# Performance work log

Measured on AMD Instinct MI355X. Metric: run time of the kernel, lower is better.

Reference implementation:

```python
import jax, jax.numpy as jnp
import numpy as np

N_HEAD = 4
D_K = 64
D_V = 64
D_MODEL = 256
LN_EPS = 1e-5


def setup_inputs() -> dict:
    key = jax.random.key(0)
    k1, k2, k3 = jax.random.split(key, 3)
    B, C, H, W = 2, D_MODEL, 64, 64
    q = jax.random.normal(k1, (B, C, H, W), dtype=jnp.float32)
    # w_qkvs: Linear(d_model, n_head*d_k, bias=False), weight [out, in]
    std_qkv = np.sqrt(2.0 / (D_MODEL + D_K))
    w_qkv = jax.random.normal(k2, (N_HEAD * D_K, D_MODEL), dtype=jnp.float32) * std_qkv
    # fc: Linear(n_head*d_v, d_model), xavier-normal-ish init
    std_fc = np.sqrt(2.0 / (N_HEAD * D_V + D_MODEL))
    fc_w = jax.random.normal(k3, (D_MODEL, N_HEAD * D_V), dtype=jnp.float32) * std_fc
    fc_b = jnp.zeros((D_MODEL,), dtype=jnp.float32)
    ln_g = jnp.ones((D_MODEL,), dtype=jnp.float32)
    ln_b = jnp.zeros((D_MODEL,), dtype=jnp.float32)
    return {"q": q, "w_qkv": w_qkv, "fc_w": fc_w, "fc_b": fc_b, "ln_g": ln_g, "ln_b": ln_b}


def reference(q, w_qkv, fc_w, fc_b, ln_g, ln_b):
    B, C, H, W = q.shape
    L = H * W
    # [B, C, H, W] -> [B, L, C]
    x = q.reshape(B, C, L).transpose(0, 2, 1)
    residual = x
    # shared QKV projection (self-attention branch: q == k == v)
    qkv = x @ w_qkv.T                                  # [B, L, nh*dk]
    qh = qkv.reshape(B, L, N_HEAD, D_K).transpose(2, 0, 1, 3)  # [h, B, L, dk]
    scale = jnp.asarray(np.sqrt(D_K), dtype=q.dtype)
    attn = jnp.einsum('hbqd,hbkd->hbqk', qh, qh) / scale       # [h, B, L, L]
    attn = jax.nn.softmax(attn, axis=-1)
    out = jnp.einsum('hbqk,hbkd->hbqd', attn, qh)              # [h, B, L, dv]
    # [h, B, L, dv] -> [B, L, h*dv]
    out = out.transpose(1, 2, 0, 3).reshape(B, L, N_HEAD * D_V)
    out = out @ fc_w.T + fc_b
    out = out + residual
    mu = jnp.mean(out, axis=-1, keepdims=True)
    var = jnp.mean(jnp.square(out - mu), axis=-1, keepdims=True)
    out = (out - mu) / jnp.sqrt(var + LN_EPS) * ln_g + ln_b
    # raw row-major view back to [B, C, H, W] (matches torch .view)
    return out.reshape(B, -1, H, W)
```

## Files before the change

### kernel.cpp

```cpp
#include <hip/hip_runtime.h>

#define L_SEQ 4096
#define DMODEL 256
#define DH 64
#define NKB 16

typedef __attribute__((ext_vector_type(8))) __bf16 bf16x8;
typedef __attribute__((ext_vector_type(4))) float f32x4;
typedef __attribute__((ext_vector_type(8))) unsigned short ushort8v;
typedef __attribute__((ext_vector_type(4))) unsigned short ushort4v;

__device__ __forceinline__ unsigned short f2bf(float f) {
  unsigned u = __builtin_bit_cast(unsigned, f);
  u += 0x7fffu + ((u >> 16) & 1u);
  return (unsigned short)(u >> 16);
}
__device__ __forceinline__ float bf2f(unsigned short h) {
  unsigned u = ((unsigned)h) << 16;
  return __builtin_bit_cast(float, u);
}
__device__ __forceinline__ bf16x8 ld_frag(const unsigned short* p) {
  return __builtin_bit_cast(bf16x8, *(const ushort8v*)p);
}

__global__ __launch_bounds__(256) void k_transpose(const float* __restrict__ q,
                                                   unsigned short* __restrict__ xbf,
                                                   const float* __restrict__ w,
                                                   const float* __restrict__ fcw,
                                                   unsigned short* __restrict__ wbf,
                                                   unsigned short* __restrict__ fcwbf) {
  int bx = blockIdx.x;
  int t = threadIdx.x;
  if (bx >= 512) {
    int i = ((bx - 512) * 256 + t) * 4;
    float4 a = *(const float4*)(w + i);
    float4 b = *(const float4*)(fcw + i);
    ushort4v av = {f2bf(a.x), f2bf(a.y), f2bf(a.z), f2bf(a.w)};
    ushort4v bv = {f2bf(b.x), f2bf(b.y), f2bf(b.z), f2bf(b.w)};
    *(ushort4v*)(wbf + i) = av;
    *(ushort4v*)(fcwbf + i) = bv;
    return;
  }
  __shared__ float T[64 * 65];
  int b = bx >> 8, rest = bx & 255;
  int ct = rest >> 6, lt = rest & 63;
#pragma unroll
  for (int it = 0; it < 4; ++it) {
    int i = (t >> 4) + it * 16;
    int j0 = (t & 15) * 4;
    float4 v = *(const float4*)(q + ((size_t)(b * 256 + ct * 64 + i)) * 4096 + lt * 64 + j0);
    T[i * 65 + j0 + 0] = v.x;
    T[i * 65 + j0 + 1] = v.y;
    T[i * 65 + j0 + 2] = v.z;
    T[i * 65 + j0 + 3] = v.w;
  }
  __syncthreads();
#pragma unroll
  for (int it = 0; it < 2; ++it) {
    int l = (t >> 3) + it * 32;
    int c0 = (t & 7) * 8;
    ushort8v o;
#pragma unroll
    for (int k = 0; k < 8; ++k) o[k] = f2bf(T[(c0 + k) * 65 + l]);
    *(ushort8v*)(xbf + ((size_t)(b * 4096 + lt * 64 + l)) * 256 + ct * 64 + c0) = o;
  }
}

#define KP2 136
__global__ __launch_bounds__(256) void k_qkv(const unsigned short* __restrict__ xbf,
                                             const unsigned short* __restrict__ wbf,
                                             unsigned short* __restrict__ Qh,
                                             unsigned short* __restrict__ QhT) {
  __shared__ unsigned short As[64 * KP2];
  __shared__ unsigned short Bs[64 * KP2];
  int bx = blockIdx.x;
  int mtile = bx >> 2, h = bx & 3;
  int m0 = mtile * 64;
  int b = m0 >> 12, l0 = m0 & 4095;
  int t = threadIdx.x;
  int wv = t >> 6, lane = t & 63, g = lane >> 4, ln = lane & 15;
  f32x4 acc[4] = {};
  for (int kb = 0; kb < 2; ++kb) {
#pragma unroll
    for (int it = 0; it < 4; ++it) {
      int idx = t + it * 256;
      int row = idx >> 4;
      int c0 = (idx & 15) * 8;
      *(ushort8v*)(As + row * KP2 + c0) =
          *(const ushort8v*)(xbf + (size_t)(m0 + row) * 256 + kb * 128 + c0);
      *(ushort8v*)(Bs + row * KP2 + c0) =
          *(const ushort8v*)(wbf + (size_t)(h * 64 + row) * 256 + kb * 128 + c0);
    }
    __syncthreads();
#pragma unroll
    for (int kc = 0; kc < 4; ++kc) {
      bf16x8 a = ld_frag(As + (wv * 16 + ln) * KP2 + kc * 32 + g * 8);
#pragma unroll
      for (int tn = 0; tn < 4; ++tn) {
        bf16x8 bb = ld_frag(Bs + (tn * 16 + ln) * KP2 + kc * 32 + g * 8);
        acc[tn] = __builtin_amdgcn_mfma_f32_16x16x32_bf16(a, bb, acc[tn], 0, 0, 0);
      }
    }
    __syncthreads();
  }
  size_t pbase = (size_t)(b * 4 + h);
#pragma unroll
  for (int tn = 0; tn < 4; ++tn) {
#pragma unroll
    for (int r = 0; r < 4; ++r) {
      int lrow = wv * 16 + g * 4 + r;
      int d = tn * 16 + ln;
      unsigned short bv = f2bf(acc[tn][r]);
      As[lrow * 64 + (((d >> 3) ^ (lrow & 7)) * 8) + (d & 7)] = bv;
      Bs[d * 64 + (((lrow >> 3) ^ (d & 7)) * 8) + (lrow & 7)] = bv;
    }
  }
#pragma unroll
  for (int s = 0; s < 2; ++s) {
    int flat = s * 64 + lane;
    int lrow = wv * 16 + (flat >> 3);
    int c8 = lane & 7;
    ushort8v v = *(const ushort8v*)(As + lrow * 64 + ((c8 ^ (lrow & 7)) * 8));
    *(ushort8v*)(Qh + (pbase * L_SEQ + l0 + lrow) * DH + c8 * 8) = v;
  }
  __syncthreads();
#pragma unroll
  for (int s = 0; s < 2; ++s) {
    int flat = s * 256 + t;
    int drow = flat >> 3;
    int c8 = t & 7;
    ushort8v v = *(const ushort8v*)(Bs + drow * 64 + ((c8 ^ (drow & 7)) * 8));
    *(ushort8v*)(QhT + (pbase * DH + drow) * L_SEQ + l0 + c8 * 8) = v;
  }
}

__global__ __launch_bounds__(256, 2) void k_attn(const unsigned short* __restrict__ Qh,
                                                 const unsigned short* __restrict__ QhT,
                                                 unsigned short* __restrict__ Opart,
                                                 float* __restrict__ Lpart) {
  __shared__ unsigned short Kt[64 * 64];
  __shared__ unsigned short Vt[64 * 64];
  __shared__ unsigned short Pb[256 * 64];
  int bx = blockIdx.x;
  int p = bx & 7;
  int u = bx >> 3;
  int qsup = u & 15, ks = u >> 4;
  int t = threadIdx.x;
  int wv = t >> 6, lane = t & 63, g = lane >> 4, ln = lane & 15;
  const unsigned short* Qp = Qh + (size_t)p * L_SEQ * DH;
  const unsigned short* QTp = QhT + (size_t)p * DH * L_SEQ;
  int q0 = qsup * 256;
  int qw = q0 + wv * 64;

  bf16x8 aQ[4][2];
#pragma unroll
  for (int nt = 0; nt < 4; ++nt)
#pragma unroll
    for (int kc = 0; kc < 2; ++kc)
      aQ[nt][kc] = ld_frag(Qp + (size_t)(qw + nt * 16 + ln) * DH + kc * 32 + g * 8);

  f32x4 oacc[4][4] = {};
  float lacc[4] = {0.f, 0.f, 0.f, 0.f};

  int srow0 = t >> 3, scol0 = t & 7;
  int srow1 = (t + 256) >> 3, scol1 = (t + 256) & 7;
  int sdst0 = srow0 * 64 + ((scol0 ^ (srow0 & 7)) * 8);
  int sdst1 = srow1 * 64 + ((scol1 ^ (srow1 & 7)) * 8);

  ushort8v kreg0, kreg1, vreg0, vreg1;
  {
    int kbase = (ks * NKB) * 64;
    kreg0 = *(const ushort8v*)(Qp + (size_t)(kbase + srow0) * DH + scol0 * 8);
    kreg1 = *(const ushort8v*)(Qp + (size_t)(kbase + srow1) * DH + scol1 * 8);
    vreg0 = *(const ushort8v*)(QTp + (size_t)srow0 * L_SEQ + kbase + scol0 * 8);
    vreg1 = *(const ushort8v*)(QTp + (size_t)srow1 * L_SEQ + kbase + scol1 * 8);
  }

  for (int kb = 0; kb < NKB; ++kb) {
    __syncthreads();
    *(ushort8v*)(Kt + sdst0) = kreg0;
    *(ushort8v*)(Kt + sdst1) = kreg1;
    *(ushort8v*)(Vt + sdst0) = vreg0;
    *(ushort8v*)(Vt + sdst1) = vreg1;
    __syncthreads();
    if (kb + 1 < NKB) {
      int kbase = (ks * NKB + kb + 1) * 64;
      kreg0 = *(const ushort8v*)(Qp + (size_t)(kbase + srow0) * DH + scol0 * 8);
      kreg1 = *(const ushort8v*)(Qp + (size_t)(kbase + srow1) * DH + scol1 * 8);
      vreg0 = *(const ushort8v*)(QTp + (size_t)srow0 * L_SEQ + kbase + scol0 * 8);
      vreg1 = *(const ushort8v*)(QTp + (size_t)srow1 * L_SEQ + kbase + scol1 * 8);
    }
#pragma unroll
    for (int mt = 0; mt < 4; ++mt) {
      int krow = mt * 16 + ln;
      bf16x8 aK0 = ld_frag(Kt + krow * 64 + (((0 * 4 + g) ^ (ln & 7)) * 8));
      bf16x8 aK1 = ld_frag(Kt + krow * 64 + (((1 * 4 + g) ^ (ln & 7)) * 8));
      f32x4 s[4] = {};
#pragma unroll
      for (int nt = 0; nt < 4; ++nt) {
        s[nt] = __builtin_amdgcn_mfma_f32_16x16x32_bf16(aK0, aQ[nt][0], s[nt], 0, 0, 0);
        s[nt] = __builtin_amdgcn_mfma_f32_16x16x32_bf16(aK1, aQ[nt][1], s[nt], 0, 0, 0);
      }
#pragma unroll
      for (int nt = 0; nt < 4; ++nt) {
        float p0 = __expf(fmaf(s[nt][0], 0.125f, -16.0f));
        float p1 = __expf(fmaf(s[nt][1], 0.125f, -16.0f));
        float p2 = __expf(fmaf(s[nt][2], 0.125f, -16.0f));
        float p3 = __expf(fmaf(s[nt][3], 0.125f, -16.0f));
        lacc[nt] += (p0 + p1) + (p2 + p3);
        ushort4v pk = {f2bf(p0), f2bf(p1), f2bf(p2), f2bf(p3)};
        int row = wv * 64 + nt * 16 + ln;
        int addr = row * 64 + (((2 * mt + (g >> 1)) ^ (ln & 7)) * 8) + (g & 1) * 4;
        *(ushort4v*)(Pb + addr) = pk;
      }
    }
#pragma unroll
    for (int kc = 0; kc < 2; ++kc) {
      bf16x8 bV[4];
#pragma unroll
      for (int tn = 0; tn < 4; ++tn)
        bV[tn] = ld_frag(Vt + (tn * 16 + ln) * 64 + (((kc * 4 + g) ^ (ln & 7)) * 8));
#pragma unroll
      for (int mq = 0; mq < 4; ++mq) {
        bf16x8 aP = ld_frag(Pb + (wv * 64 + mq * 16 + ln) * 64 + (((kc * 4 + g) ^ (ln & 7)) * 8));
#pragma unroll
        for (int tn = 0; tn < 4; ++tn)
          oacc[mq][tn] = __builtin_amdgcn_mfma_f32_16x16x32_bf16(aP, bV[tn], oacc[mq][tn], 0, 0, 0);
      }
    }
  }
#pragma unroll
  for (int nt = 0; nt < 4; ++nt) {
    lacc[nt] += __shfl_xor(lacc[nt], 16, 64);
    lacc[nt] += __shfl_xor(lacc[nt], 32, 64);
  }
  size_t pq = (size_t)(ks * 8 + p) * L_SEQ;
  if (g == 0) {
#pragma unroll
    for (int nt = 0; nt < 4; ++nt)
      __builtin_nontemporal_store(lacc[nt], &Lpart[pq + qw + nt * 16 + ln]);
  }
#pragma unroll
  for (int mq = 0; mq < 4; ++mq) {
#pragma unroll
    for (int r = 0; r < 4; ++r) {
      int row = wv * 64 + mq * 16 + g * 4 + r;
#pragma unroll
      for (int tn = 0; tn < 4; ++tn) {
        int d = tn * 16 + ln;
        Pb[row * 64 + (((d >> 3) ^ (row & 7)) * 8) + (d & 7)] = f2bf(oacc[mq][tn][r]);
      }
    }
  }
#pragma unroll
  for (int s = 0; s < 8; ++s) {
    int flat = s * 64 + lane;
    int row = wv * 64 + (flat >> 3);
    int c8 = lane & 7;
    ushort8v v = *(const ushort8v*)(Pb + row * 64 + ((c8 ^ (row & 7)) * 8));
    __builtin_nontemporal_store(v, (ushort8v*)(Opart + (pq + q0 + row) * DH + c8 * 8));
  }
}

#define CP 72
__global__ __launch_bounds__(256) void k_fc(const unsigned short* __restrict__ Opart,
                                            const float* __restrict__ Lpart,
                                            const unsigned short* __restrict__ fcwbf,
                                            const float* __restrict__ qres,
                                            const float* __restrict__ fcb,
                                            const float* __restrict__ lng,
                                            const float* __restrict__ lnb,
                                            float* __restrict__ out) {
  __shared__ unsigned short As[32 * CP];
  __shared__ unsigned short Bs[256 * CP];
  __shared__ float redS[4][32], redQ[4][32], muA[32], rsA[32];
  int bx = blockIdx.x;
  int m0 = bx * 32;
  int b = m0 >> 12, lpart = m0 & 4095;
  int t = threadIdx.x;
  int wv = t >> 6, lane = t & 63, g = lane >> 4, ln = lane & 15;
  f32x4 acc[2][4] = {};
  for (int kb = 0; kb < 4; ++kb) {
    {
      int row = t >> 3, c0 = (t & 7) * 8;
      int q = lpart + row;
      int p = b * 4 + kb;
      float lsum = __builtin_nontemporal_load(&Lpart[(size_t)(0 * 8 + p) * L_SEQ + q]) +
                   __builtin_nontemporal_load(&Lpart[(size_t)(1 * 8 + p) * L_SEQ + q]) +
                   __builtin_nontemporal_load(&Lpart[(size_t)(2 * 8 + p) * L_SEQ + q]) +
                   __builtin_nontemporal_load(&Lpart[(size_t)(3 * 8 + p) * L_SEQ + q]);
      float inv = 1.0f / lsum;
      float a8[8] = {0.f, 0.f, 0.f, 0.f, 0.f, 0.f, 0.f, 0.f};
#pragma unroll
      for (int ksp = 0; ksp < 4; ++ksp) {
        ushort8v v = __builtin_nontemporal_load(
            (const ushort8v*)(Opart + ((size_t)(ksp * 8 + p) * L_SEQ + q) * DH + c0));
#pragma unroll
        for (int j = 0; j < 8; ++j) a8[j] += bf2f(v[j]);
      }
      ushort8v o;
#pragma unroll
      for (int j = 0; j < 8; ++j) o[j] = f2bf(a8[j] * inv);
      *(ushort8v*)(As + row * CP + c0) = o;
    }
#pragma unroll
    for (int it = 0; it < 8; ++it) {
      int idx = t + it * 256;
      int row = idx >> 3, c0 = (idx & 7) * 8;
      *(ushort8v*)(Bs + row * CP + c0) =
          *(const ushort8v*)(fcwbf + (size_t)row * 256 + kb * 64 + c0);
    }
    __syncthreads();
#pragma unroll
    for (int kc = 0; kc < 2; ++kc) {
      bf16x8 a[2], bb[4];
#pragma unroll
      for (int mt = 0; mt < 2; ++mt) a[mt] = ld_frag(As + (mt * 16 + ln) * CP + kc * 32 + g * 8);
#pragma unroll
      for (int tn = 0; tn < 4; ++tn) bb[tn] = ld_frag(Bs + (wv * 64 + tn * 16 + ln) * CP + kc * 32 + g * 8);
#pragma unroll
      for (int mt = 0; mt < 2; ++mt)
#pragma unroll
        for (int tn = 0; tn < 4; ++tn)
          acc[mt][tn] = __builtin_amdgcn_mfma_f32_16x16x32_bf16(a[mt], bb[tn], acc[mt][tn], 0, 0, 0);
    }
    __syncthreads();
  }
  float fb[4], lg[4], lb[4];
#pragma unroll
  for (int tn = 0; tn < 4; ++tn) {
    int o = wv * 64 + tn * 16 + ln;
    fb[tn] = fcb[o]; lg[tn] = lng[o]; lb[tn] = lnb[o];
  }
#pragma unroll
  for (int mt = 0; mt < 2; ++mt) {
    float ps[4] = {0.f, 0.f, 0.f, 0.f}, pq2[4] = {0.f, 0.f, 0.f, 0.f};
#pragma unroll
    for (int tn = 0; tn < 4; ++tn) {
      int o = wv * 64 + tn * 16 + ln;
      float4 res = *(const float4*)(qres + ((size_t)(b * 256 + o)) * 4096 + lpart + mt * 16 + g * 4);
      float rv[4] = {res.x, res.y, res.z, res.w};
#pragma unroll
      for (int r = 0; r < 4; ++r) {
        float v = acc[mt][tn][r] + fb[tn] + rv[r];
        acc[mt][tn][r] = v;
        ps[r] += v;
        pq2[r] += v * v;
      }
    }
#pragma unroll
    for (int r = 0; r < 4; ++r) {
      float s = ps[r], q2 = pq2[r];
#pragma unroll
      for (int off = 1; off < 16; off <<= 1) {
        s += __shfl_xor(s, off, 64);
        q2 += __shfl_xor(q2, off, 64);
      }
      if (ln == 0) {
        int row = mt * 16 + g * 4 + r;
        redS[wv][row] = s;
        redQ[wv][row] = q2;
      }
    }
  }
  __syncthreads();
  if (t < 32) {
    float s = redS[0][t] + redS[1][t] + redS[2][t] + redS[3][t];
    float q2 = redQ[0][t] + redQ[1][t] + redQ[2][t] + redQ[3][t];
    float mu = s * (1.f / 256.f);
    float var = q2 * (1.f / 256.f) - mu * mu;
    muA[t] = mu;
    rsA[t] = rsqrtf(var + 1e-5f);
  }
  __syncthreads();
#pragma unroll
  for (int mt = 0; mt < 2; ++mt) {
#pragma unroll
    for (int r = 0; r < 4; ++r) {
      int row = mt * 16 + g * 4 + r;
      float mu = muA[row], rs = rsA[row];
#pragma unroll
      for (int tn = 0; tn < 4; ++tn) {
        int o = wv * 64 + tn * 16 + ln;
        out[(size_t)(m0 + row) * 256 + o] = (acc[mt][tn][r] - mu) * rs * lg[tn] + lb[tn];
      }
    }
  }
}

extern "C" void kernel_launch(void* const* d_in, const int* in_sizes, int n_in,
                              void* d_out, int out_size, void* d_ws, size_t ws_size,
                              hipStream_t stream) {
  const float* q = (const float*)d_in[0];
  const float* w_qkv = (const float*)d_in[1];
  const float* fc_w = (const float*)d_in[2];
  const float* fc_b = (const float*)d_in[3];
  const float* ln_g = (const float*)d_in[4];
  const float* ln_b = (const float*)d_in[5];
  float* out = (float*)d_out;

  unsigned short* wbf = (unsigned short*)d_ws;
  unsigned short* fcwbf = wbf + 65536;
  unsigned short* xbf = fcwbf + 65536;
  unsigned short* Qh = xbf + 2097152;
  unsigned short* QhT = Qh + 2097152;
  unsigned short* Opart = QhT + 2097152;
  float* Lpart = (float*)(Opart + 8388608);

  k_transpose<<<dim3(576), dim3(256), 0, stream>>>(q, xbf, w_qkv, fc_w, wbf, fcwbf);
  k_qkv<<<dim3(512), dim3(256), 0, stream>>>(xbf, wbf, Qh, QhT);
  k_attn<<<dim3(512), dim3(256), 0, stream>>>(Qh, QhT, Opart, Lpart);
  k_fc<<<dim3(256), dim3(256), 0, stream>>>(Opart, Lpart, fcwbf, q, fc_b, ln_g, ln_b, out);
}
```

Measured before the change: 140.6 us.

## Switch attention to 32x32 MFMA with register-resident P and double-buffered K/V

The attention kernel moves from 16x16x32 to 32x32x16 bf16 MFMA tiles and computes S transposed so the exponentiated probabilities can be packed with v_cvt_pk_bf16_f32 and rearranged with v_permlane32_swap. They then feed the PV MFMA directly from registers, with no round trip through a shared-memory P buffer. K/V tiles are double-buffered in LDS, which removes one barrier per iteration. The output is written straight from the accumulators as packed bf16, with no LDS transpose staging. This aims to cut LDS traffic and barriers, at the cost of relying on gfx950-specific instructions and a more intricate register layout.

Result: slower. 151.1 us (+7.4%).

```diff
diff --git a/kernel.cpp b/kernel.cpp
--- a/kernel.cpp
+++ b/kernel.cpp
@@ -7,8 +7,11 @@
 
 typedef __attribute__((ext_vector_type(8))) __bf16 bf16x8;
 typedef __attribute__((ext_vector_type(4))) float f32x4;
+typedef __attribute__((ext_vector_type(16))) float f32x16;
 typedef __attribute__((ext_vector_type(8))) unsigned short ushort8v;
 typedef __attribute__((ext_vector_type(4))) unsigned short ushort4v;
+typedef __attribute__((ext_vector_type(2))) unsigned int uint2v;
+typedef __attribute__((ext_vector_type(4))) unsigned int uint4v;
 
 __device__ __forceinline__ unsigned short f2bf(float f) {
   unsigned u = __builtin_bit_cast(unsigned, f);
@@ -21,6 +24,14 @@
 }
 __device__ __forceinline__ bf16x8 ld_frag(const unsigned short* p) {
   return __builtin_bit_cast(bf16x8, *(const ushort8v*)p);
+}
+__device__ __forceinline__ unsigned cvtpk(float lo, float hi) {
+  unsigned r;
+  asm("v_cvt_pk_bf16_f32 %0, %1, %2" : "=v"(r) : "v"(lo), "v"(hi));
+  return r;
+}
+__device__ __forceinline__ void plswap(unsigned& a, unsigned& b) {
+  asm("v_permlane32_swap_b32 %0, %1" : "+v"(a), "+v"(b));
 }
 
 __global__ __launch_bounds__(256) void k_transpose(const float* __restrict__ q,
@@ -138,128 +149,123 @@
                                                  const unsigned short* __restrict__ QhT,
                                                  unsigned short* __restrict__ Opart,
                                                  float* __restrict__ Lpart) {
-  __shared__ unsigned short Kt[64 * 64];
-  __shared__ unsigned short Vt[64 * 64];
-  __shared__ unsigned short Pb[256 * 64];
+  __shared__ unsigned short smem[4 * 4096];
   int bx = blockIdx.x;
   int p = bx & 7;
   int u = bx >> 3;
   int qsup = u & 15, ks = u >> 4;
   int t = threadIdx.x;
-  int wv = t >> 6, lane = t & 63, g = lane >> 4, ln = lane & 15;
+  int wv = t >> 6, lane = t & 63, ln = lane & 31, hi = lane >> 5;
   const unsigned short* Qp = Qh + (size_t)p * L_SEQ * DH;
   const unsigned short* QTp = QhT + (size_t)p * DH * L_SEQ;
   int q0 = qsup * 256;
   int qw = q0 + wv * 64;
 
-  bf16x8 aQ[4][2];
-#pragma unroll
-  for (int nt = 0; nt < 4; ++nt)
-#pragma unroll
-    for (int kc = 0; kc < 2; ++kc)
-      aQ[nt][kc] = ld_frag(Qp + (size_t)(qw + nt * 16 + ln) * DH + kc * 32 + g * 8);
-
-  f32x4 oacc[4][4] = {};
-  float lacc[4] = {0.f, 0.f, 0.f, 0.f};
-
-  int srow0 = t >> 3, scol0 = t & 7;
-  int srow1 = (t + 256) >> 3, scol1 = (t + 256) & 7;
-  int sdst0 = srow0 * 64 + ((scol0 ^ (srow0 & 7)) * 8);
-  int sdst1 = srow1 * 64 + ((scol1 ^ (srow1 & 7)) * 8);
+  bf16x8 aQ[2][4];
+#pragma unroll
+  for (int qt = 0; qt < 2; ++qt)
+#pragma unroll
+    for (int kq = 0; kq < 4; ++kq)
+      aQ[qt][kq] = ld_frag(Qp + (size_t)(qw + qt * 32 + ln) * DH + kq * 16 + hi * 8);
+
+  f32x16 oacc[2][2] = {};
+  float lacc[2] = {0.f, 0.f};
+
+  int srow0 = t >> 3, scol = t & 7;
+  int srow1 = srow0 + 32;
+  int sdst0 = srow0 * 64 + ((scol ^ (srow0 & 7)) * 8);
+  int sdst1 = srow1 * 64 + ((scol ^ (srow1 & 7)) * 8);
 
   ushort8v kreg0, kreg1, vreg0, vreg1;
   {
     int kbase = (ks * NKB) * 64;
-    kreg0 = *(const ushort8v*)(Qp + (size_t)(kbase + srow0) * DH + scol0 * 8);
-    kreg1 = *(const ushort8v*)(Qp + (size_t)(kbase + srow1) * DH + scol1 * 8);
-    vreg0 = *(const ushort8v*)(QTp + (size_t)srow0 * L_SEQ + kbase + scol0 * 8);
-    vreg1 = *(const ushort8v*)(QTp + (size_t)srow1 * L_SEQ + kbase + scol1 * 8);
+    kreg0 = *(const ushort8v*)(Qp + (size_t)(kbase + srow0) * DH + scol * 8);
+    kreg1 = *(const ushort8v*)(Qp + (size_t)(kbase + srow1) * DH + scol * 8);
+    vreg0 = *(const ushort8v*)(QTp + (size_t)srow0 * L_SEQ + kbase + scol * 8);
+    vreg1 = *(const ushort8v*)(QTp + (size_t)srow1 * L_SEQ + kbase + scol * 8);
   }
 
   for (int kb = 0; kb < NKB; ++kb) {
-    __syncthreads();
-    *(ushort8v*)(Kt + sdst0) = kreg0;
-    *(ushort8v*)(Kt + sdst1) = kreg1;
-    *(ushort8v*)(Vt + sdst0) = vreg0;
-    *(ushort8v*)(Vt + sdst1) = vreg1;
+    unsigned short* Kc = smem + (kb & 1) * 8192;
+    unsigned short* Vc = Kc + 4096;
+    *(ushort8v*)(Kc + sdst0) = kreg0;
+    *(ushort8v*)(Kc + sdst1) = kreg1;
+    *(ushort8v*)(Vc + sdst0) = vreg0;
+    *(ushort8v*)(Vc + sdst1) = vreg1;
     __syncthreads();
     if (kb + 1 < NKB) {
       int kbase = (ks * NKB + kb + 1) * 64;
-      kreg0 = *(const ushort8v*)(Qp + (size_t)(kbase + srow0) * DH + scol0 * 8);
-      kreg1 = *(const ushort8v*)(Qp + (size_t)(kbase + srow1) * DH + scol1 * 8);
-      vreg0 = *(const ushort8v*)(QTp + (size_t)srow0 * L_SEQ + kbase + scol0 * 8);
-      vreg1 = *(const ushort8v*)(QTp + (size_t)srow1 * L_SEQ + kbase + scol1 * 8);
-    }
-#pragma unroll
-    for (int mt = 0; mt < 4; ++mt) {
-      int krow = mt * 16 + ln;
-      bf16x8 aK0 = ld_frag(Kt + krow * 64 + (((0 * 4 + g) ^ (ln & 7)) * 8));
-      bf16x8 aK1 = ld_frag(Kt + krow * 64 + (((1 * 4 + g) ^ (ln & 7)) * 8));
-      f32x4 s[4] = {};
-#pragma unroll
-      for (int nt = 0; nt < 4; ++nt) {
-        s[nt] = __builtin_amdgcn_mfma_f32_16x16x32_bf16(aK0, aQ[nt][0], s[nt], 0, 0, 0);
-        s[nt] = __builtin_amdgcn_mfma_f32_16x16x32_bf16(aK1, aQ[nt][1], s[nt], 0, 0, 0);
-      }
-#pragma unroll
-      for (int nt = 0; nt < 4; ++nt) {
-        float p0 = __expf(fmaf(s[nt][0], 0.125f, -16.0f));
-        float p1 = __expf(fmaf(s[nt][1], 0.125f, -16.0f));
-        float p2 = __expf(fmaf(s[nt][2], 0.125f, -16.0f));
-        float p3 = __expf(fmaf(s[nt][3], 0.125f, -16.0f));
-        lacc[nt] += (p0 + p1) + (p2 + p3);
-        ushort4v pk = {f2bf(p0), f2bf(p1), f2bf(p2), f2bf(p3)};
-        int row = wv * 64 + nt * 16 + ln;
-        int addr = row * 64 + (((2 * mt + (g >> 1)) ^ (ln & 7)) * 8) + (g & 1) * 4;
-        *(ushort4v*)(Pb + addr) = pk;
-      }
-    }
-#pragma unroll
-    for (int kc = 0; kc < 2; ++kc) {
-      bf16x8 bV[4];
-#pragma unroll
-      for (int tn = 0; tn < 4; ++tn)
-        bV[tn] = ld_frag(Vt + (tn * 16 + ln) * 64 + (((kc * 4 + g) ^ (ln & 7)) * 8));
-#pragma unroll
-      for (int mq = 0; mq < 4; ++mq) {
-        bf16x8 aP = ld_frag(Pb + (wv * 64 + mq * 16 + ln) * 64 + (((kc * 4 + g) ^ (ln & 7)) * 8));
-#pragma unroll
-        for (int tn = 0; tn < 4; ++tn)
-          oacc[mq][tn] = __builtin_amdgcn_mfma_f32_16x16x32_bf16(aP, bV[tn], oacc[mq][tn], 0, 0, 0);
-      }
-    }
-  }
-#pragma unroll
-  for (int nt = 0; nt < 4; ++nt) {
-    lacc[nt] += __shfl_xor(lacc[nt], 16, 64);
-    lacc[nt] += __shfl_xor(lacc[nt], 32, 64);
-  }
+      kreg0 = *(const ushort8v*)(Qp + (size_t)(kbase + srow0) * DH + scol * 8);
+      kreg1 = *(const ushort8v*)(Qp + (size_t)(kbase + srow1) * DH + scol * 8);
+      vreg0 = *(const ushort8v*)(QTp + (size_t)srow0 * L_SEQ + kbase + scol * 8);
+      vreg1 = *(const ushort8v*)(QTp + (size_t)srow1 * L_SEQ + kbase + scol * 8);
+    }
+#pragma unroll
+    for (int mt = 0; mt < 2; ++mt) {
+      int key = mt * 32 + ln;
+      bf16x8 aK[4];
+#pragma unroll
+      for (int kq = 0; kq < 4; ++kq)
+        aK[kq] = ld_frag(Kc + key * 64 + (((kq * 2 + hi) ^ (key & 7)) * 8));
+      bf16x8 pf[2][2];
+#pragma unroll
+      for (int qt = 0; qt < 2; ++qt) {
+        f32x16 s = {};
+#pragma unroll
+        for (int kq = 0; kq < 4; ++kq)
+          s = __builtin_amdgcn_mfma_f32_32x32x16_bf16(aK[kq], aQ[qt][kq], s, 0, 0, 0);
+        float pv[16];
+#pragma unroll
+        for (int r = 0; r < 16; ++r) pv[r] = __expf(fmaf(s[r], 0.125f, -16.0f));
+        lacc[qt] += (((pv[0] + pv[1]) + (pv[2] + pv[3])) + ((pv[4] + pv[5]) + (pv[6] + pv[7]))) +
+                    (((pv[8] + pv[9]) + (pv[10] + pv[11])) + ((pv[12] + pv[13]) + (pv[14] + pv[15])));
+        unsigned w0 = cvtpk(pv[0], pv[1]), w1 = cvtpk(pv[2], pv[3]);
+        unsigned w2 = cvtpk(pv[4], pv[5]), w3 = cvtpk(pv[6], pv[7]);
+        unsigned w4 = cvtpk(pv[8], pv[9]), w5 = cvtpk(pv[10], pv[11]);
+        unsigned w6 = cvtpk(pv[12], pv[13]), w7 = cvtpk(pv[14], pv[15]);
+        plswap(w0, w2);
+        plswap(w1, w3);
+        plswap(w4, w6);
+        plswap(w5, w7);
+        uint4v c0 = {w0, w1, w2, w3};
+        uint4v c1 = {w4, w5, w6, w7};
+        pf[qt][0] = __builtin_bit_cast(bf16x8, c0);
+        pf[qt][1] = __builtin_bit_cast(bf16x8, c1);
+      }
+#pragma unroll
+      for (int dt = 0; dt < 2; ++dt) {
+        int d = dt * 32 + ln;
+        bf16x8 vf[2];
+#pragma unroll
+        for (int c = 0; c < 2; ++c)
+          vf[c] = ld_frag(Vc + d * 64 + (((mt * 4 + c * 2 + hi) ^ (d & 7)) * 8));
+#pragma unroll
+        for (int qt = 0; qt < 2; ++qt)
+#pragma unroll
+          for (int c = 0; c < 2; ++c)
+            oacc[dt][qt] = __builtin_amdgcn_mfma_f32_32x32x16_bf16(vf[c], pf[qt][c], oacc[dt][qt], 0, 0, 0);
+      }
+    }
+  }
+#pragma unroll
+  for (int qt = 0; qt < 2; ++qt) lacc[qt] += __shfl_xor(lacc[qt], 32, 64);
   size_t pq = (size_t)(ks * 8 + p) * L_SEQ;
-  if (g == 0) {
-#pragma unroll
-    for (int nt = 0; nt < 4; ++nt)
-      __builtin_nontemporal_store(lacc[nt], &Lpart[pq + qw + nt * 16 + ln]);
-  }
-#pragma unroll
-  for (int mq = 0; mq < 4; ++mq) {
-#pragma unroll
-    for (int r = 0; r < 4; ++r) {
-      int row = wv * 64 + mq * 16 + g * 4 + r;
-#pragma unroll
-      for (int tn = 0; tn < 4; ++tn) {
-        int d = tn * 16 + ln;
-        Pb[row * 64 + (((d >> 3) ^ (row & 7)) * 8) + (d & 7)] = f2bf(oacc[mq][tn][r]);
-      }
-    }
-  }
-#pragma unroll
-  for (int s = 0; s < 8; ++s) {
-    int flat = s * 64 + lane;
-    int row = wv * 64 + (flat >> 3);
-    int c8 = lane & 7;
-    ushort8v v = *(const ushort8v*)(Pb + row * 64 + ((c8 ^ (row & 7)) * 8));
-    __builtin_nontemporal_store(v, (ushort8v*)(Opart + (pq + q0 + row) * DH + c8 * 8));
-  }
+  if (lane < 32) {
+    __builtin_nontemporal_store(lacc[0], &Lpart[pq + qw + ln]);
+    __builtin_nontemporal_store(lacc[1], &Lpart[pq + qw + 32 + ln]);
+  }
+#pragma unroll
+  for (int dt = 0; dt < 2; ++dt)
+#pragma unroll
+    for (int qt = 0; qt < 2; ++qt) {
+      size_t rb = (pq + qw + qt * 32 + ln) * DH + dt * 32 + hi * 4;
+#pragma unroll
+      for (int g8 = 0; g8 < 4; ++g8) {
+        uint2v wv2 = {cvtpk(oacc[dt][qt][g8 * 4 + 0], oacc[dt][qt][g8 * 4 + 1]),
+                      cvtpk(oacc[dt][qt][g8 * 4 + 2], oacc[dt][qt][g8 * 4 + 3])};
+        __builtin_nontemporal_store(wv2, (uint2v*)(Opart + rb + g8 * 8));
+      }
+    }
 }
 
 #define CP 72
```
